# Optimization experiments

Hardware: AMD Instinct MI355X
Metric: run time of the kernel (lower is better)

## Reference

```python
import jax, jax.numpy as jnp
import numpy as np
from jax import lax

M = 4      # signature truncation depth (init kwarg m)
D = 6      # path channel dimension
L = 100000 # path length


def _kron(a, b):
    # flat tensor product of two flattened tensor levels
    return (a[:, None] * b[None, :]).ravel()


def signature(x, m):
    """Truncated path signature of x (L, d) up to depth m, flat concat of levels.
    Matches iisignature.sig(x, m): output size d + d^2 + ... + d^m.
    Sequential Chen recursion over path increments via lax.scan."""
    d = x.shape[1]
    dx = x[1:] - x[:-1]  # (L-1, d) increments

    def step(S, v):
        # exp of the linear segment: e[k] = v^{(x)k} / k!
        e = [v]
        for k in range(2, m + 1):
            e.append(_kron(e[-1], v) / k)
        # Chen: S'^k = S^k + e^k + sum_{j=1}^{k-1} S^j (x) e^{k-j}
        newS = []
        for k in range(1, m + 1):
            t = S[k - 1] + e[k - 1]
            for j in range(1, k):
                t = t + _kron(S[j - 1], e[k - 1 - j])
            newS.append(t)
        return tuple(newS), None

    S0 = tuple(jnp.zeros((d ** k,), x.dtype) for k in range(1, m + 1))
    S, _ = lax.scan(step, S0, dx)
    return jnp.concatenate(S)  # (d + d^2 + ... + d^m,)


def setup_inputs() -> dict:
    key = jax.random.key(0)
    # build a realistic path: cumulative sum of small Gaussian increments
    steps = jax.random.normal(key, (L, D), dtype=jnp.float32) * 0.01
    x = jnp.cumsum(steps, axis=0)
    return {"x": x}


def reference(x) -> jnp.ndarray:
    return signature(x, M)
```

## Files before the change

kernel.cpp:

```cpp
#include <hip/hip_runtime.h>

#define SIGSZ 1554
#define PSTRIDE 1600
#define OFF4 0
#define OFF3 1296
#define OFF2 1512
#define OFF1 1548
#define MAXROWS 80

#define REP6(M) M(0) M(1) M(2) M(3) M(4) M(5)
#define REP6B(M, k) M(k, 0) M(k, 1) M(k, 2) M(k, 3) M(k, 4) M(k, 5)
#define REP36(M) \
  REP6B(M, 0) REP6B(M, 1) REP6B(M, 2) REP6B(M, 3) REP6B(M, 4) REP6B(M, 5)

__device__ __forceinline__ float sel6(int idx, float a0, float a1, float a2,
                                      float a3, float a4, float a5) {
  float r = a0;
  r = (idx == 1) ? a1 : r;
  r = (idx == 2) ? a2 : r;
  r = (idx == 3) ? a3 : r;
  r = (idx == 4) ? a4 : r;
  r = (idx == 5) ? a5 : r;
  return r;
}

__global__ __launch_bounds__(64, 1) void sig_chunk(const float* __restrict__ x,
                                                   float* __restrict__ out,
                                                   int n_inc, int chunk_len) {
  __shared__ float xs[MAXROWS * 6];
  const int c = blockIdx.x;
  const int p = threadIdx.x;
  const int t0 = c * chunk_len;
  int t1 = t0 + chunk_len; if (t1 > n_inc) t1 = n_inc;
  const int steps = (t1 > t0) ? (t1 - t0) : 0;
  const int pc = (p < 36) ? p : 35;
  const int i = pc / 6, j = pc % 6;
  const bool act = (p < 36);

  const int nfl = (steps > 0) ? (steps + 1) * 6 : 0;
  for (int idx = p; idx < nfl; idx += 64) xs[idx] = x[(size_t)t0 * 6 + idx];
  __syncthreads();

#define DECL_S4(k, l) float s4_##k##_##l = 0.f;
  REP36(DECL_S4)
#undef DECL_S4
#define DECL_S3(k) float s3_##k = 0.f;
  REP6(DECL_S3)
#undef DECL_S3
  float s1i = 0.f, s2 = 0.f;

  float cr0 = 0, cr1 = 0, cr2 = 0, cr3 = 0, cr4 = 0, cr5 = 0;
  float nr0 = 0, nr1 = 0, nr2 = 0, nr3 = 0, nr4 = 0, nr5 = 0;
  if (steps > 0) {
    const float2* q0 = (const float2*)(xs);
    float2 a0 = q0[0], b0 = q0[1], d0 = q0[2];
    cr0 = a0.x; cr1 = a0.y; cr2 = b0.x; cr3 = b0.y; cr4 = d0.x; cr5 = d0.y;
    const float2* q1 = (const float2*)(xs + 6);
    float2 a1 = q1[0], b1 = q1[1], d1 = q1[2];
    nr0 = a1.x; nr1 = a1.y; nr2 = b1.x; nr3 = b1.y; nr4 = d1.x; nr5 = d1.y;
  }

  for (int r = 0; r < steps; ++r) {
    const float v0 = nr0 - cr0, v1 = nr1 - cr1, v2 = nr2 - cr2;
    const float v3 = nr3 - cr3, v4 = nr4 - cr4, v5 = nr5 - cr5;

    int ro = r + 2; ro = (ro > steps) ? steps : ro;
    const float2* qp = (const float2*)(xs + ro * 6);
    const float2 pa = qp[0], pb = qp[1], pd = qp[2];

    const float vi = sel6(i, v0, v1, v2, v3, v4, v5);
    const float vj = sel6(j, v0, v1, v2, v3, v4, v5);
    const float aa = vi * vj;
    const float sv = s1i * vj;
    const float G2  = fmaf(aa, 1.f / 6.f,  fmaf(sv, 0.5f,      s2));
    const float in4 = fmaf(aa, 1.f / 24.f, fmaf(sv, 1.f / 6.f, s2 * 0.5f));
#define MKG(k)                                    \
    const float G_##k = fmaf(in4, v##k, s3_##k);  \
    s3_##k = fmaf(G2, v##k, s3_##k);
    REP6(MKG)
#undef MKG
#define UPD4(k, l) s4_##k##_##l = fmaf(G_##k, v##l, s4_##k##_##l);
    REP36(UPD4)
#undef UPD4
    s2 = fmaf(fmaf(vi, 0.5f, s1i), vj, s2);
    s1i += vi;

    cr0 = nr0; cr1 = nr1; cr2 = nr2; cr3 = nr3; cr4 = nr4; cr5 = nr5;
    nr0 = pa.x; nr1 = pa.y; nr2 = pb.x; nr3 = pb.y; nr4 = pd.x; nr5 = pd.y;
  }

  float* st = out + (size_t)c * PSTRIDE;
  if (act) {
    float4* o4 = (float4*)(st + OFF4 + pc * 36);
    float4 w;
    w.x = s4_0_0; w.y = s4_0_1; w.z = s4_0_2; w.w = s4_0_3; o4[0] = w;
    w.x = s4_0_4; w.y = s4_0_5; w.z = s4_1_0; w.w = s4_1_1; o4[1] = w;
    w.x = s4_1_2; w.y = s4_1_3; w.z = s4_1_4; w.w = s4_1_5; o4[2] = w;
    w.x = s4_2_0; w.y = s4_2_1; w.z = s4_2_2; w.w = s4_2_3; o4[3] = w;
    w.x = s4_2_4; w.y = s4_2_5; w.z = s4_3_0; w.w = s4_3_1; o4[4] = w;
    w.x = s4_3_2; w.y = s4_3_3; w.z = s4_3_4; w.w = s4_3_5; o4[5] = w;
    w.x = s4_4_0; w.y = s4_4_1; w.z = s4_4_2; w.w = s4_4_3; o4[6] = w;
    w.x = s4_4_4; w.y = s4_4_5; w.z = s4_5_0; w.w = s4_5_1; o4[7] = w;
    w.x = s4_5_2; w.y = s4_5_3; w.z = s4_5_4; w.w = s4_5_5; o4[8] = w;
#define ST3(k) st[OFF3 + pc * 6 + k] = s3_##k;
    REP6(ST3)
#undef ST3
    st[OFF2 + pc] = s2;
    if (j == 0) st[OFF1 + i] = s1i;
  }
}


#define DECLSET(S)                                                  \
  float S##b4_0, S##b4_1, S##b4_2, S##b4_3, S##b4_4, S##b4_5;       \
  float S##b3r_0, S##b3r_1, S##b3r_2, S##b3r_3, S##b3r_4, S##b3r_5; \
  float S##b2r_0, S##b2r_1, S##b2r_2, S##b2r_3, S##b2r_4, S##b2r_5; \
  float S##b1_0, S##b1_1, S##b1_2, S##b1_3, S##b1_4, S##b1_5;       \
  float S##b2ij, S##b2jk, S##b3ijk, S##b1k, S##b1j;

#define LOADSET(S, bp) {                                            \
  const float2* q4 = (const float2*)((bp) + oB4);                   \
  float2 u0 = q4[0], u1 = q4[1], u2 = q4[2];                        \
  S##b4_0 = u0.x; S##b4_1 = u0.y; S##b4_2 = u1.x;                   \
  S##b4_3 = u1.y; S##b4_4 = u2.x; S##b4_5 = u2.y;                   \
  const float2* q3 = (const float2*)((bp) + oB3r);                  \
  float2 w0 = q3[0], w1 = q3[1], w2 = q3[2];                        \
  S##b3r_0 = w0.x; S##b3r_1 = w0.y; S##b3r_2 = w1.x;                \
  S##b3r_3 = w1.y; S##b3r_4 = w2.x; S##b3r_5 = w2.y;                \
  const float2* q2 = (const float2*)((bp) + oB2r);                  \
  float2 y0 = q2[0], y1 = q2[1], y2 = q2[2];                        \
  S##b2r_0 = y0.x; S##b2r_1 = y0.y; S##b2r_2 = y1.x;                \
  S##b2r_3 = y1.y; S##b2r_4 = y2.x; S##b2r_5 = y2.y;                \
  const float2* q1 = (const float2*)((bp) + OFF1);                  \
  float2 z0 = q1[0], z1 = q1[1], z2 = q1[2];                        \
  S##b1_0 = z0.x; S##b1_1 = z0.y; S##b1_2 = z1.x;                   \
  S##b1_3 = z1.y; S##b1_4 = z2.x; S##b1_5 = z2.y;                   \
  S##b2ij = (bp)[oB2ij]; S##b2jk = (bp)[oB2jk];                     \
  S##b3ijk = (bp)[oB3ijk];                                          \
  S##b1k = (bp)[oB1k]; S##b1j = (bp)[oB1j];                         \
}

#define PROD(S) {                                                   \
  const float a1i = sel6(i_, a1_0, a1_1, a1_2, a1_3, a1_4, a1_5);   \
  a4_0 = fmaf(a3, S##b1_0, fmaf(a2, S##b2r_0,                       \
         fmaf(a1i, S##b3r_0, a4_0 + S##b4_0)));                     \
  a4_1 = fmaf(a3, S##b1_1, fmaf(a2, S##b2r_1,                       \
         fmaf(a1i, S##b3r_1, a4_1 + S##b4_1)));                     \
  a4_2 = fmaf(a3, S##b1_2, fmaf(a2, S##b2r_2,                       \
         fmaf(a1i, S##b3r_2, a4_2 + S##b4_2)));                     \
  a4_3 = fmaf(a3, S##b1_3, fmaf(a2, S##b2r_3,                       \
         fmaf(a1i, S##b3r_3, a4_3 + S##b4_3)));                     \
  a4_4 = fmaf(a3, S##b1_4, fmaf(a2, S##b2r_4,                       \
         fmaf(a1i, S##b3r_4, a4_4 + S##b4_4)));                     \
  a4_5 = fmaf(a3, S##b1_5, fmaf(a2, S##b2r_5,                       \
         fmaf(a1i, S##b3r_5, a4_5 + S##b4_5)));                     \
  a3 = fmaf(a2, S##b1k, fmaf(a1i, S##b2jk, a3 + S##b3ijk));         \
  a2 = fmaf(a1i, S##b1j, a2 + S##b2ij);                             \
  a1_0 += S##b1_0; a1_1 += S##b1_1; a1_2 += S##b1_2;                \
  a1_3 += S##b1_3; a1_4 += S##b1_4; a1_5 += S##b1_5;                \
}

__global__ __launch_bounds__(256, 1) void sig_combine(const float* __restrict__ in,
                                                      float* __restrict__ out,
                                                      int n_total, int group,
                                                      int final_out) {
  const int b = blockIdx.x;
  const int p = threadIdx.x;
  const int start = b * group;
  int end = start + group; if (end > n_total) end = n_total;
  const int tc = (p < 216) ? p : 215;
  const bool act = (p < 216);
  const int k_ = tc % 6;
  const int ij = tc / 6;
  const int j_ = ij % 6;
  const int i_ = ij / 6;

  const int oB4 = OFF4 + tc * 6;
  const int oB3r = OFF3 + (j_ * 6 + k_) * 6;
  const int oB2r = OFF2 + k_ * 6;
  const int oB2ij = OFF2 + ij;
  const int oB2jk = OFF2 + j_ * 6 + k_;
  const int oB3ijk = OFF3 + tc;
  const int oB1k = OFF1 + k_;
  const int oB1j = OFF1 + j_;

  const float* sp0 = in + (size_t)start * PSTRIDE;
  float a4_0, a4_1, a4_2, a4_3, a4_4, a4_5;
  {
    const float2* q4 = (const float2*)(sp0 + oB4);
    float2 u0 = q4[0], u1 = q4[1], u2 = q4[2];
    a4_0 = u0.x; a4_1 = u0.y; a4_2 = u1.x;
    a4_3 = u1.y; a4_4 = u2.x; a4_5 = u2.y;
  }
  float a3 = sp0[oB3ijk];
  float a2 = sp0[oB2ij];
  float a1_0, a1_1, a1_2, a1_3, a1_4, a1_5;
  {
    const float2* q1 = (const float2*)(sp0 + OFF1);
    float2 z0 = q1[0], z1 = q1[1], z2 = q1[2];
    a1_0 = z0.x; a1_1 = z0.y; a1_2 = z1.x;
    a1_3 = z1.y; a1_4 = z2.x; a1_5 = z2.y;
  }

  DECLSET(A)
  DECLSET(B)

  int s = start + 1;
  {
    const int sa = (s < end) ? s : (end - 1);
    LOADSET(A, in + (size_t)sa * PSTRIDE)
    const int sb = (s + 1 < end) ? (s + 1) : (end - 1);
    LOADSET(B, in + (size_t)sb * PSTRIDE)
  }
  while (s + 1 < end) {
    PROD(A)
    {
      const int sn = (s + 2 < end) ? (s + 2) : (end - 1);
      LOADSET(A, in + (size_t)sn * PSTRIDE)
    }
    PROD(B)
    {
      const int sn = (s + 3 < end) ? (s + 3) : (end - 1);
      LOADSET(B, in + (size_t)sn * PSTRIDE)
    }
    s += 2;
  }
  if (s < end) { PROD(A) }

  const float a1p = sel6(p, a1_0, a1_1, a1_2, a1_3, a1_4, a1_5);
  if (final_out) {
    float* o = out;
    if (act) {
      float2* o2 = (float2*)(o + 258 + tc * 6);
      float2 w;
      w.x = a4_0; w.y = a4_1; o2[0] = w;
      w.x = a4_2; w.y = a4_3; o2[1] = w;
      w.x = a4_4; w.y = a4_5; o2[2] = w;
      o[42 + tc] = a3;
      if (k_ == 0) o[6 + ij] = a2;
    }
    if (p < 6) o[p] = a1p;
  } else {
    float* st = out + (size_t)b * PSTRIDE;
    if (act) {
      float2* o2 = (float2*)(st + oB4);
      float2 w;
      w.x = a4_0; w.y = a4_1; o2[0] = w;
      w.x = a4_2; w.y = a4_3; o2[1] = w;
      w.x = a4_4; w.y = a4_5; o2[2] = w;
      st[oB3ijk] = a3;
      if (k_ == 0) st[oB2ij] = a2;
    }
    if (p < 6) st[OFF1 + p] = a1p;
  }
}

extern "C" void kernel_launch(void* const* d_in, const int* in_sizes, int n_in,
                              void* d_out, int out_size, void* d_ws, size_t ws_size,
                              hipStream_t stream) {
  const float* x = (const float*)d_in[0];
  const int Lrows = in_sizes[0] / 6;
  const int n_inc = Lrows - 1;

  int P = 2048;
  int chunk_len = (n_inc + P - 1) / P;
  if (chunk_len > MAXROWS - 1) {
    chunk_len = MAXROWS - 1;
    P = (n_inc + chunk_len - 1) / chunk_len;
  }

  float* ws0 = (float*)d_ws;
  float* ws1 = ws0 + (size_t)P * PSTRIDE;

  sig_chunk<<<P, 64, 0, stream>>>(x, ws0, n_inc, chunk_len);

  float* cur = ws0;
  float* other = ws1;
  int n = P;
  while (n > 1) {
    const int g = (n <= 16) ? n : 16;
    const int nb = (n + g - 1) / g;
    const int fin = (nb == 1);
    sig_combine<<<nb, 256, 0, stream>>>(cur, fin ? (float*)d_out : other, n, g, fin);
    float* t = cur; cur = other; other = t;
    n = nb;
  }
}
```

Baseline: 94.54 us.

## Fuse combine tree into single last-block kernel and raise chunk count

Raises the chunk count from 2048 to up to 4096 with shorter chunks. The chunk kernel now precomputes increments into shared memory, unrolls the step loop by two, and allows more blocks per CU. The multi-launch combine tree becomes one kernel: each 1024-thread block combines 64 states in four subgroups merged through LDS, and the last block to finish, found with an atomic counter, combines the block results into the output. This removes several kernel launches and adds more parallel work, at the cost of atomics, fences, and the final reduction running in one block.

```diff
diff --git a/kernel.cpp b/kernel.cpp
--- a/kernel.cpp
+++ b/kernel.cpp
@@ -6,12 +6,8 @@
 #define OFF3 1296
 #define OFF2 1512
 #define OFF1 1548
-#define MAXROWS 80
-
-#define REP6(M) M(0) M(1) M(2) M(3) M(4) M(5)
-#define REP6B(M, k) M(k, 0) M(k, 1) M(k, 2) M(k, 3) M(k, 4) M(k, 5)
-#define REP36(M) \
-  REP6B(M, 0) REP6B(M, 1) REP6B(M, 2) REP6B(M, 3) REP6B(M, 4) REP6B(M, 5)
+#define VROWS 64
+#define PMAX 4096
 
 __device__ __forceinline__ float sel6(int idx, float a0, float a1, float a2,
                                       float a3, float a4, float a5) {
@@ -24,12 +20,43 @@
   return r;
 }
 
-__global__ __launch_bounds__(64, 1) void sig_chunk(const float* __restrict__ x,
+#define DECL4ROW(k) float s4_##k##_0 = 0.f, s4_##k##_1 = 0.f, s4_##k##_2 = 0.f, \
+                          s4_##k##_3 = 0.f, s4_##k##_4 = 0.f, s4_##k##_5 = 0.f;
+
+#define LOADROW(S, row) { \
+  const float2* q_ = (const float2*)(vs + (row) * 6); \
+  const float2 a_ = q_[0], b_ = q_[1], d_ = q_[2]; \
+  S##v0 = a_.x; S##v1 = a_.y; S##v2 = b_.x; \
+  S##v3 = b_.y; S##v4 = d_.x; S##v5 = d_.y; \
+  S##vi = vs[(row) * 6 + i]; S##vj = vs[(row) * 6 + j]; \
+}
+
+#define MKG_S(S, k) const float G##S##k = fmaf(in4, S##v##k, s3_##k); \
+                    s3_##k = fmaf(G2, S##v##k, s3_##k);
+#define UPD_S(S, k, l) s4_##k##_##l = fmaf(G##S##k, S##v##l, s4_##k##_##l);
+#define UPDROW_S(S, k) UPD_S(S,k,0) UPD_S(S,k,1) UPD_S(S,k,2) \
+                       UPD_S(S,k,3) UPD_S(S,k,4) UPD_S(S,k,5)
+
+#define STEP(S) { \
+  const float aa = S##vi * S##vj; \
+  const float sv = s1i * S##vj; \
+  const float G2 = fmaf(aa, 1.f / 6.f, fmaf(sv, 0.5f, s2)); \
+  const float in4 = fmaf(aa, 1.f / 24.f, fmaf(sv, 1.f / 6.f, s2 * 0.5f)); \
+  MKG_S(S,0) MKG_S(S,1) MKG_S(S,2) MKG_S(S,3) MKG_S(S,4) MKG_S(S,5) \
+  UPDROW_S(S,0) UPDROW_S(S,1) UPDROW_S(S,2) \
+  UPDROW_S(S,3) UPDROW_S(S,4) UPDROW_S(S,5) \
+  s2 = fmaf(fmaf(S##vi, 0.5f, s1i), S##vj, s2); \
+  s1i += S##vi; \
+}
+
+__global__ __launch_bounds__(64, 4) void sig_chunk(const float* __restrict__ x,
                                                    float* __restrict__ out,
+                                                   unsigned* __restrict__ counter,
                                                    int n_inc, int chunk_len) {
-  __shared__ float xs[MAXROWS * 6];
+  __shared__ alignas(16) float vs[VROWS * 6];
   const int c = blockIdx.x;
   const int p = threadIdx.x;
+  if (c == 0 && p == 0) *counter = 0u;
   const int t0 = c * chunk_len;
   int t1 = t0 + chunk_len; if (t1 > n_inc) t1 = n_inc;
   const int steps = (t1 > t0) ? (t1 - t0) : 0;
@@ -37,56 +64,26 @@
   const int i = pc / 6, j = pc % 6;
   const bool act = (p < 36);
 
-  const int nfl = (steps > 0) ? (steps + 1) * 6 : 0;
-  for (int idx = p; idx < nfl; idx += 64) xs[idx] = x[(size_t)t0 * 6 + idx];
+  const int nv = steps * 6;
+  const float* xb = x + (size_t)t0 * 6;
+  for (int idx = p; idx < nv; idx += 64) vs[idx] = xb[idx + 6] - xb[idx];
+  for (int idx = nv + p; idx < nv + 18; idx += 64) vs[idx] = 0.f;
   __syncthreads();
 
-#define DECL_S4(k, l) float s4_##k##_##l = 0.f;
-  REP36(DECL_S4)
-#undef DECL_S4
-#define DECL_S3(k) float s3_##k = 0.f;
-  REP6(DECL_S3)
-#undef DECL_S3
+  DECL4ROW(0) DECL4ROW(1) DECL4ROW(2) DECL4ROW(3) DECL4ROW(4) DECL4ROW(5)
+  float s3_0 = 0.f, s3_1 = 0.f, s3_2 = 0.f, s3_3 = 0.f, s3_4 = 0.f, s3_5 = 0.f;
   float s1i = 0.f, s2 = 0.f;
 
-  float cr0 = 0, cr1 = 0, cr2 = 0, cr3 = 0, cr4 = 0, cr5 = 0;
-  float nr0 = 0, nr1 = 0, nr2 = 0, nr3 = 0, nr4 = 0, nr5 = 0;
-  if (steps > 0) {
-    const float2* q0 = (const float2*)(xs);
-    float2 a0 = q0[0], b0 = q0[1], d0 = q0[2];
-    cr0 = a0.x; cr1 = a0.y; cr2 = b0.x; cr3 = b0.y; cr4 = d0.x; cr5 = d0.y;
-    const float2* q1 = (const float2*)(xs + 6);
-    float2 a1 = q1[0], b1 = q1[1], d1 = q1[2];
-    nr0 = a1.x; nr1 = a1.y; nr2 = b1.x; nr3 = b1.y; nr4 = d1.x; nr5 = d1.y;
-  }
-
-  for (int r = 0; r < steps; ++r) {
-    const float v0 = nr0 - cr0, v1 = nr1 - cr1, v2 = nr2 - cr2;
-    const float v3 = nr3 - cr3, v4 = nr4 - cr4, v5 = nr5 - cr5;
-
-    int ro = r + 2; ro = (ro > steps) ? steps : ro;
-    const float2* qp = (const float2*)(xs + ro * 6);
-    const float2 pa = qp[0], pb = qp[1], pd = qp[2];
-
-    const float vi = sel6(i, v0, v1, v2, v3, v4, v5);
-    const float vj = sel6(j, v0, v1, v2, v3, v4, v5);
-    const float aa = vi * vj;
-    const float sv = s1i * vj;
-    const float G2  = fmaf(aa, 1.f / 6.f,  fmaf(sv, 0.5f,      s2));
-    const float in4 = fmaf(aa, 1.f / 24.f, fmaf(sv, 1.f / 6.f, s2 * 0.5f));
-#define MKG(k)                                    \
-    const float G_##k = fmaf(in4, v##k, s3_##k);  \
-    s3_##k = fmaf(G2, v##k, s3_##k);
-    REP6(MKG)
-#undef MKG
-#define UPD4(k, l) s4_##k##_##l = fmaf(G_##k, v##l, s4_##k##_##l);
-    REP36(UPD4)
-#undef UPD4
-    s2 = fmaf(fmaf(vi, 0.5f, s1i), vj, s2);
-    s1i += vi;
-
-    cr0 = nr0; cr1 = nr1; cr2 = nr2; cr3 = nr3; cr4 = nr4; cr5 = nr5;
-    nr0 = pa.x; nr1 = pa.y; nr2 = pb.x; nr3 = pb.y; nr4 = pd.x; nr5 = pd.y;
+  float Av0, Av1, Av2, Av3, Av4, Av5, Avi, Avj;
+  float Bv0, Bv1, Bv2, Bv3, Bv4, Bv5, Bvi, Bvj;
+  LOADROW(A, 0)
+  LOADROW(B, 1)
+  const int steps_up = (steps + 1) & ~1;
+  for (int r = 0; r < steps_up; r += 2) {
+    STEP(A)
+    LOADROW(A, r + 2)
+    STEP(B)
+    LOADROW(B, r + 3)
   }
 
   float* st = out + (size_t)c * PSTRIDE;
@@ -102,14 +99,44 @@
     w.x = s4_4_0; w.y = s4_4_1; w.z = s4_4_2; w.w = s4_4_3; o4[6] = w;
     w.x = s4_4_4; w.y = s4_4_5; w.z = s4_5_0; w.w = s4_5_1; o4[7] = w;
     w.x = s4_5_2; w.y = s4_5_3; w.z = s4_5_4; w.w = s4_5_5; o4[8] = w;
-#define ST3(k) st[OFF3 + pc * 6 + k] = s3_##k;
-    REP6(ST3)
-#undef ST3
+    st[OFF3 + pc * 6 + 0] = s3_0;
+    st[OFF3 + pc * 6 + 1] = s3_1;
+    st[OFF3 + pc * 6 + 2] = s3_2;
+    st[OFF3 + pc * 6 + 3] = s3_3;
+    st[OFF3 + pc * 6 + 4] = s3_4;
+    st[OFF3 + pc * 6 + 5] = s3_5;
     st[OFF2 + pc] = s2;
     if (j == 0) st[OFF1 + i] = s1i;
   }
 }
 
+struct Acc {
+  float a4_0, a4_1, a4_2, a4_3, a4_4, a4_5;
+  float a3, a2;
+  float a1_0, a1_1, a1_2, a1_3, a1_4, a1_5;
+};
+
+struct Lane {
+  int i_, j_, k_, ij, tc;
+  int oB4, oB3r, oB2r, oB2ij, oB2jk, oB3ijk, oB1k, oB1j;
+  bool act;
+};
+
+__device__ __forceinline__ Lane make_lane(int pl) {
+  Lane L;
+  const int tc = (pl < 216) ? pl : 215;
+  L.tc = tc; L.act = (pl < 216);
+  L.k_ = tc % 6; L.ij = tc / 6; L.j_ = L.ij % 6; L.i_ = L.ij / 6;
+  L.oB4 = OFF4 + tc * 6;
+  L.oB3r = OFF3 + (L.j_ * 6 + L.k_) * 6;
+  L.oB2r = OFF2 + L.k_ * 6;
+  L.oB2ij = OFF2 + L.ij;
+  L.oB2jk = OFF2 + L.j_ * 6 + L.k_;
+  L.oB3ijk = OFF3 + tc;
+  L.oB1k = OFF1 + L.k_;
+  L.oB1j = OFF1 + L.j_;
+  return L;
+}
 
 #define DECLSET(S)                                                  \
   float S##b4_0, S##b4_1, S##b4_2, S##b4_3, S##b4_4, S##b4_5;       \
@@ -119,139 +146,175 @@
   float S##b2ij, S##b2jk, S##b3ijk, S##b1k, S##b1j;
 
 #define LOADSET(S, bp) {                                            \
-  const float2* q4 = (const float2*)((bp) + oB4);                   \
-  float2 u0 = q4[0], u1 = q4[1], u2 = q4[2];                        \
+  const float2* q4 = (const float2*)((bp) + L.oB4);                 \
+  const float2 u0 = q4[0], u1 = q4[1], u2 = q4[2];                  \
   S##b4_0 = u0.x; S##b4_1 = u0.y; S##b4_2 = u1.x;                   \
   S##b4_3 = u1.y; S##b4_4 = u2.x; S##b4_5 = u2.y;                   \
-  const float2* q3 = (const float2*)((bp) + oB3r);                  \
-  float2 w0 = q3[0], w1 = q3[1], w2 = q3[2];                        \
+  const float2* q3 = (const float2*)((bp) + L.oB3r);                \
+  const float2 w0 = q3[0], w1 = q3[1], w2 = q3[2];                  \
   S##b3r_0 = w0.x; S##b3r_1 = w0.y; S##b3r_2 = w1.x;                \
   S##b3r_3 = w1.y; S##b3r_4 = w2.x; S##b3r_5 = w2.y;                \
-  const float2* q2 = (const float2*)((bp) + oB2r);                  \
-  float2 y0 = q2[0], y1 = q2[1], y2 = q2[2];                        \
+  const float2* q2 = (const float2*)((bp) + L.oB2r);                \
+  const float2 y0 = q2[0], y1 = q2[1], y2 = q2[2];                  \
   S##b2r_0 = y0.x; S##b2r_1 = y0.y; S##b2r_2 = y1.x;                \
   S##b2r_3 = y1.y; S##b2r_4 = y2.x; S##b2r_5 = y2.y;                \
   const float2* q1 = (const float2*)((bp) + OFF1);                  \
-  float2 z0 = q1[0], z1 = q1[1], z2 = q1[2];                        \
+  const float2 z0 = q1[0], z1 = q1[1], z2 = q1[2];                  \
   S##b1_0 = z0.x; S##b1_1 = z0.y; S##b1_2 = z1.x;                   \
   S##b1_3 = z1.y; S##b1_4 = z2.x; S##b1_5 = z2.y;                   \
-  S##b2ij = (bp)[oB2ij]; S##b2jk = (bp)[oB2jk];                     \
-  S##b3ijk = (bp)[oB3ijk];                                          \
-  S##b1k = (bp)[oB1k]; S##b1j = (bp)[oB1j];                         \
+  S##b2ij = (bp)[L.oB2ij]; S##b2jk = (bp)[L.oB2jk];                 \
+  S##b3ijk = (bp)[L.oB3ijk];                                        \
+  S##b1k = (bp)[L.oB1k]; S##b1j = (bp)[L.oB1j];                     \
 }
 
 #define PROD(S) {                                                   \
-  const float a1i = sel6(i_, a1_0, a1_1, a1_2, a1_3, a1_4, a1_5);   \
-  a4_0 = fmaf(a3, S##b1_0, fmaf(a2, S##b2r_0,                       \
-         fmaf(a1i, S##b3r_0, a4_0 + S##b4_0)));                     \
-  a4_1 = fmaf(a3, S##b1_1, fmaf(a2, S##b2r_1,                       \
-         fmaf(a1i, S##b3r_1, a4_1 + S##b4_1)));                     \
-  a4_2 = fmaf(a3, S##b1_2, fmaf(a2, S##b2r_2,                       \
-         fmaf(a1i, S##b3r_2, a4_2 + S##b4_2)));                     \
-  a4_3 = fmaf(a3, S##b1_3, fmaf(a2, S##b2r_3,                       \
-         fmaf(a1i, S##b3r_3, a4_3 + S##b4_3)));                     \
-  a4_4 = fmaf(a3, S##b1_4, fmaf(a2, S##b2r_4,                       \
-         fmaf(a1i, S##b3r_4, a4_4 + S##b4_4)));                     \
-  a4_5 = fmaf(a3, S##b1_5, fmaf(a2, S##b2r_5,                       \
-         fmaf(a1i, S##b3r_5, a4_5 + S##b4_5)));                     \
-  a3 = fmaf(a2, S##b1k, fmaf(a1i, S##b2jk, a3 + S##b3ijk));         \
-  a2 = fmaf(a1i, S##b1j, a2 + S##b2ij);                             \
-  a1_0 += S##b1_0; a1_1 += S##b1_1; a1_2 += S##b1_2;                \
-  a1_3 += S##b1_3; a1_4 += S##b1_4; a1_5 += S##b1_5;                \
-}
-
-__global__ __launch_bounds__(256, 1) void sig_combine(const float* __restrict__ in,
-                                                      float* __restrict__ out,
-                                                      int n_total, int group,
-                                                      int final_out) {
-  const int b = blockIdx.x;
-  const int p = threadIdx.x;
-  const int start = b * group;
-  int end = start + group; if (end > n_total) end = n_total;
-  const int tc = (p < 216) ? p : 215;
-  const bool act = (p < 216);
-  const int k_ = tc % 6;
-  const int ij = tc / 6;
-  const int j_ = ij % 6;
-  const int i_ = ij / 6;
-
-  const int oB4 = OFF4 + tc * 6;
-  const int oB3r = OFF3 + (j_ * 6 + k_) * 6;
-  const int oB2r = OFF2 + k_ * 6;
-  const int oB2ij = OFF2 + ij;
-  const int oB2jk = OFF2 + j_ * 6 + k_;
-  const int oB3ijk = OFF3 + tc;
-  const int oB1k = OFF1 + k_;
-  const int oB1j = OFF1 + j_;
-
-  const float* sp0 = in + (size_t)start * PSTRIDE;
-  float a4_0, a4_1, a4_2, a4_3, a4_4, a4_5;
+  const float a1i = sel6(L.i_, acc.a1_0, acc.a1_1, acc.a1_2,        \
+                         acc.a1_3, acc.a1_4, acc.a1_5);             \
+  acc.a4_0 = fmaf(acc.a3, S##b1_0, fmaf(acc.a2, S##b2r_0,           \
+             fmaf(a1i, S##b3r_0, acc.a4_0 + S##b4_0)));             \
+  acc.a4_1 = fmaf(acc.a3, S##b1_1, fmaf(acc.a2, S##b2r_1,           \
+             fmaf(a1i, S##b3r_1, acc.a4_1 + S##b4_1)));             \
+  acc.a4_2 = fmaf(acc.a3, S##b1_2, fmaf(acc.a2, S##b2r_2,           \
+             fmaf(a1i, S##b3r_2, acc.a4_2 + S##b4_2)));             \
+  acc.a4_3 = fmaf(acc.a3, S##b1_3, fmaf(acc.a2, S##b2r_3,           \
+             fmaf(a1i, S##b3r_3, acc.a4_3 + S##b4_3)));             \
+  acc.a4_4 = fmaf(acc.a3, S##b1_4, fmaf(acc.a2, S##b2r_4,           \
+             fmaf(a1i, S##b3r_4, acc.a4_4 + S##b4_4)));             \
+  acc.a4_5 = fmaf(acc.a3, S##b1_5, fmaf(acc.a2, S##b2r_5,           \
+             fmaf(a1i, S##b3r_5, acc.a4_5 + S##b4_5)));             \
+  acc.a3 = fmaf(acc.a2, S##b1k, fmaf(a1i, S##b2jk, acc.a3 + S##b3ijk)); \
+  acc.a2 = fmaf(a1i, S##b1j, acc.a2 + S##b2ij);                     \
+  acc.a1_0 += S##b1_0; acc.a1_1 += S##b1_1; acc.a1_2 += S##b1_2;    \
+  acc.a1_3 += S##b1_3; acc.a1_4 += S##b1_4; acc.a1_5 += S##b1_5;    \
+}
+
+__device__ __forceinline__ Acc combine_span(const float* base, int first,
+                                            int cnt, const Lane& L) {
+  Acc acc = {};
+  if (cnt <= 0) return acc;
+  const float* sp0 = base + (size_t)first * PSTRIDE;
   {
-    const float2* q4 = (const float2*)(sp0 + oB4);
-    float2 u0 = q4[0], u1 = q4[1], u2 = q4[2];
-    a4_0 = u0.x; a4_1 = u0.y; a4_2 = u1.x;
-    a4_3 = u1.y; a4_4 = u2.x; a4_5 = u2.y;
-  }
-  float a3 = sp0[oB3ijk];
-  float a2 = sp0[oB2ij];
-  float a1_0, a1_1, a1_2, a1_3, a1_4, a1_5;
+    const float2* q4 = (const float2*)(sp0 + L.oB4);
+    const float2 u0 = q4[0], u1 = q4[1], u2 = q4[2];
+    acc.a4_0 = u0.x; acc.a4_1 = u0.y; acc.a4_2 = u1.x;
+    acc.a4_3 = u1.y; acc.a4_4 = u2.x; acc.a4_5 = u2.y;
+    acc.a3 = sp0[L.oB3ijk];
+    acc.a2 = sp0[L.oB2ij];
+    const float2* q1 = (const float2*)(sp0 + OFF1);
+    const float2 z0 = q1[0], z1 = q1[1], z2 = q1[2];
+    acc.a1_0 = z0.x; acc.a1_1 = z0.y; acc.a1_2 = z1.x;
+    acc.a1_3 = z1.y; acc.a1_4 = z2.x; acc.a1_5 = z2.y;
+  }
+  if (cnt == 1) return acc;
+  DECLSET(X)
+  DECLSET(Y)
+  const int end = first + cnt;
+  int s = first + 1;
   {
-    const float2* q1 = (const float2*)(sp0 + OFF1);
-    float2 z0 = q1[0], z1 = q1[1], z2 = q1[2];
-    a1_0 = z0.x; a1_1 = z0.y; a1_2 = z1.x;
-    a1_3 = z1.y; a1_4 = z2.x; a1_5 = z2.y;
-  }
-
-  DECLSET(A)
-  DECLSET(B)
-
-  int s = start + 1;
-  {
-    const int sa = (s < end) ? s : (end - 1);
-    LOADSET(A, in + (size_t)sa * PSTRIDE)
+    LOADSET(X, base + (size_t)s * PSTRIDE)
     const int sb = (s + 1 < end) ? (s + 1) : (end - 1);
-    LOADSET(B, in + (size_t)sb * PSTRIDE)
+    LOADSET(Y, base + (size_t)sb * PSTRIDE)
   }
   while (s + 1 < end) {
-    PROD(A)
+    PROD(X)
     {
       const int sn = (s + 2 < end) ? (s + 2) : (end - 1);
-      LOADSET(A, in + (size_t)sn * PSTRIDE)
+      LOADSET(X, base + (size_t)sn * PSTRIDE)
     }
-    PROD(B)
+    PROD(Y)
     {
       const int sn = (s + 3 < end) ? (s + 3) : (end - 1);
-      LOADSET(B, in + (size_t)sn * PSTRIDE)
+      LOADSET(Y, base + (size_t)sn * PSTRIDE)
     }
     s += 2;
   }
-  if (s < end) { PROD(A) }
-
-  const float a1p = sel6(p, a1_0, a1_1, a1_2, a1_3, a1_4, a1_5);
-  if (final_out) {
-    float* o = out;
-    if (act) {
-      float2* o2 = (float2*)(o + 258 + tc * 6);
-      float2 w;
-      w.x = a4_0; w.y = a4_1; o2[0] = w;
-      w.x = a4_2; w.y = a4_3; o2[1] = w;
-      w.x = a4_4; w.y = a4_5; o2[2] = w;
-      o[42 + tc] = a3;
-      if (k_ == 0) o[6 + ij] = a2;
+  if (s < end) { PROD(X) }
+  return acc;
+}
+
+__device__ __forceinline__ void apply_state(Acc& acc, const float* bp,
+                                            const Lane& L) {
+  DECLSET(Z)
+  LOADSET(Z, bp)
+  PROD(Z)
+}
+
+__device__ __forceinline__ void store_partial(float* st, const Acc& acc,
+                                              const Lane& L, int pl) {
+  if (L.act) {
+    float2* o2 = (float2*)(st + L.oB4);
+    float2 w;
+    w.x = acc.a4_0; w.y = acc.a4_1; o2[0] = w;
+    w.x = acc.a4_2; w.y = acc.a4_3; o2[1] = w;
+    w.x = acc.a4_4; w.y = acc.a4_5; o2[2] = w;
+    st[L.oB3ijk] = acc.a3;
+    if (L.k_ == 0) st[L.oB2ij] = acc.a2;
+  }
+  if (pl < 6)
+    st[OFF1 + pl] = sel6(pl, acc.a1_0, acc.a1_1, acc.a1_2,
+                         acc.a1_3, acc.a1_4, acc.a1_5);
+}
+
+__device__ __forceinline__ void store_final(float* o, const Acc& acc,
+                                            const Lane& L, int pl) {
+  if (L.act) {
+    float2* o2 = (float2*)(o + 258 + L.tc * 6);
+    float2 w;
+    w.x = acc.a4_0; w.y = acc.a4_1; o2[0] = w;
+    w.x = acc.a4_2; w.y = acc.a4_3; o2[1] = w;
+    w.x = acc.a4_4; w.y = acc.a4_5; o2[2] = w;
+    o[42 + L.tc] = acc.a3;
+    if (L.k_ == 0) o[6 + L.ij] = acc.a2;
+  }
+  if (pl < 6)
+    o[pl] = sel6(pl, acc.a1_0, acc.a1_1, acc.a1_2,
+                 acc.a1_3, acc.a1_4, acc.a1_5);
+}
+
+__global__ __launch_bounds__(1024) void sig_combine_all(
+    const float* __restrict__ in, float* __restrict__ mid,
+    float* __restrict__ out, unsigned* __restrict__ counter, int n_total) {
+  __shared__ alignas(16) float lds[3 * PSTRIDE];
+  __shared__ unsigned s_last;
+  const int pl = threadIdx.x & 255;
+  const int sub = threadIdx.x >> 8;
+  const Lane L = make_lane(pl);
+
+  {
+    const int gs = blockIdx.x * 64 + sub * 16;
+    int gc = n_total - gs; if (gc > 16) gc = 16;
+    Acc acc = combine_span(in, gs, gc, L);
+    if (sub != 0) store_partial(lds + (size_t)(sub - 1) * PSTRIDE, acc, L, pl);
+    __syncthreads();
+    if (sub == 0) {
+      apply_state(acc, lds + 0 * PSTRIDE, L);
+      apply_state(acc, lds + 1 * PSTRIDE, L);
+      apply_state(acc, lds + 2 * PSTRIDE, L);
+      store_partial(mid + (size_t)blockIdx.x * PSTRIDE, acc, L, pl);
     }
-    if (p < 6) o[p] = a1p;
-  } else {
-    float* st = out + (size_t)b * PSTRIDE;
-    if (act) {
-      float2* o2 = (float2*)(st + oB4);
-      float2 w;
-      w.x = a4_0; w.y = a4_1; o2[0] = w;
-      w.x = a4_2; w.y = a4_3; o2[1] = w;
-      w.x = a4_4; w.y = a4_5; o2[2] = w;
-      st[oB3ijk] = a3;
-      if (k_ == 0) st[oB2ij] = a2;
+  }
+
+  __threadfence();
+  __syncthreads();
+  if (threadIdx.x == 0)
+    s_last = (atomicAdd(counter, 1u) == (unsigned)(gridDim.x - 1)) ? 1u : 0u;
+  __syncthreads();
+  if (!s_last) return;
+  __threadfence();
+
+  {
+    const int gs = sub * 16;
+    int gc = (int)gridDim.x - gs; if (gc > 16) gc = 16;
+    Acc acc = combine_span(mid, gs, gc, L);
+    __syncthreads();
+    if (sub != 0) store_partial(lds + (size_t)(sub - 1) * PSTRIDE, acc, L, pl);
+    __syncthreads();
+    if (sub == 0) {
+      apply_state(acc, lds + 0 * PSTRIDE, L);
+      apply_state(acc, lds + 1 * PSTRIDE, L);
+      apply_state(acc, lds + 2 * PSTRIDE, L);
+      store_final(out, acc, L, pl);
     }
-    if (p < 6) st[OFF1 + p] = a1p;
   }
 }
 
@@ -262,27 +325,19 @@
   const int Lrows = in_sizes[0] / 6;
   const int n_inc = Lrows - 1;
 
-  int P = 2048;
+  int P = PMAX;
   int chunk_len = (n_inc + P - 1) / P;
-  if (chunk_len > MAXROWS - 1) {
-    chunk_len = MAXROWS - 1;
+  if (chunk_len > VROWS - 3) {
+    chunk_len = VROWS - 3;
     P = (n_inc + chunk_len - 1) / chunk_len;
   }
 
   float* ws0 = (float*)d_ws;
-  float* ws1 = ws0 + (size_t)P * PSTRIDE;
-
-  sig_chunk<<<P, 64, 0, stream>>>(x, ws0, n_inc, chunk_len);
-
-  float* cur = ws0;
-  float* other = ws1;
-  int n = P;
-  while (n > 1) {
-    const int g = (n <= 16) ? n : 16;
-    const int nb = (n + g - 1) / g;
-    const int fin = (nb == 1);
-    sig_combine<<<nb, 256, 0, stream>>>(cur, fin ? (float*)d_out : other, n, g, fin);
-    float* t = cur; cur = other; other = t;
-    n = nb;
-  }
-}
+  float* ws1 = ws0 + (size_t)PMAX * PSTRIDE;
+  unsigned* counter = (unsigned*)(ws1 + (size_t)64 * PSTRIDE);
+
+  sig_chunk<<<P, 64, 0, stream>>>(x, ws0, counter, n_inc, chunk_len);
+
+  const int nb = (P + 63) / 64;
+  sig_combine_all<<<nb, 1024, 0, stream>>>(ws0, ws1, (float*)d_out, counter, P);
+}
```

After: 135.5 us. +43.3%, slower.

## Vectorize chunk kernel with packed float2 FMAs, precomputed increments, more chunks

Applied to the files above, without the earlier changes.

The chunk kernel now computes increments once into shared memory and updates the level-3 and level-4 accumulators with packed two-wide FMAs. It also replaces the six-way select with direct LDS indexing and unrolls the step loop by two using double-buffered row loads. The chunk count doubles from 2048 to 4096 so chunks are shorter, and launch bounds allow four blocks per unit. The aim is fewer VALU instructions per step and more parallelism, paid for with a larger combine tree and more partial-signature traffic through the workspace.

```diff
diff --git a/kernel.cpp b/kernel.cpp
--- a/kernel.cpp
+++ b/kernel.cpp
@@ -6,12 +6,17 @@
 #define OFF3 1296
 #define OFF2 1512
 #define OFF1 1548
-#define MAXROWS 80
-
-#define REP6(M) M(0) M(1) M(2) M(3) M(4) M(5)
-#define REP6B(M, k) M(k, 0) M(k, 1) M(k, 2) M(k, 3) M(k, 4) M(k, 5)
-#define REP36(M) \
-  REP6B(M, 0) REP6B(M, 1) REP6B(M, 2) REP6B(M, 3) REP6B(M, 4) REP6B(M, 5)
+#define VROWS 64
+#define PMAX 4096
+
+typedef float v2f __attribute__((ext_vector_type(2)));
+
+__device__ __forceinline__ v2f vfma2(v2f a, v2f b, v2f c) {
+  return __builtin_elementwise_fma(a, b, c);
+}
+__device__ __forceinline__ v2f splat2(float s) {
+  v2f r; r.x = s; r.y = s; return r;
+}
 
 __device__ __forceinline__ float sel6(int idx, float a0, float a1, float a2,
                                       float a3, float a4, float a5) {
@@ -24,10 +29,44 @@
   return r;
 }
 
-__global__ __launch_bounds__(64, 1) void sig_chunk(const float* __restrict__ x,
+#define DECL4ROW(k) v2f s4_##k##_0 = {0.f, 0.f}, s4_##k##_1 = {0.f, 0.f}, \
+                        s4_##k##_2 = {0.f, 0.f};
+
+#define LOADROW(S, row) { \
+  const v2f* q_ = (const v2f*)(vs + (row) * 6); \
+  S##p0 = q_[0]; S##p1 = q_[1]; S##p2 = q_[2]; \
+  S##vi = vs[(row) * 6 + i]; S##vj = vs[(row) * 6 + j]; \
+}
+
+#define UPD4K(S, k, gk) { \
+  const v2f gk2 = splat2(gk); \
+  s4_##k##_0 = vfma2(gk2, S##p0, s4_##k##_0); \
+  s4_##k##_1 = vfma2(gk2, S##p1, s4_##k##_1); \
+  s4_##k##_2 = vfma2(gk2, S##p2, s4_##k##_2); \
+}
+
+#define STEP(S) { \
+  const float aa = S##vi * S##vj; \
+  const float sv = s1i * S##vj; \
+  const float G2 = fmaf(aa, 1.f / 6.f, fmaf(sv, 0.5f, s2)); \
+  const float in4 = fmaf(aa, 1.f / 24.f, fmaf(sv, 1.f / 6.f, s2 * 0.5f)); \
+  const v2f in42 = splat2(in4), G22 = splat2(G2); \
+  const v2f Gp0 = vfma2(in42, S##p0, s3p0); \
+  const v2f Gp1 = vfma2(in42, S##p1, s3p1); \
+  const v2f Gp2 = vfma2(in42, S##p2, s3p2); \
+  s3p0 = vfma2(G22, S##p0, s3p0); \
+  s3p1 = vfma2(G22, S##p1, s3p1); \
+  s3p2 = vfma2(G22, S##p2, s3p2); \
+  UPD4K(S, 0, Gp0.x) UPD4K(S, 1, Gp0.y) UPD4K(S, 2, Gp1.x) \
+  UPD4K(S, 3, Gp1.y) UPD4K(S, 4, Gp2.x) UPD4K(S, 5, Gp2.y) \
+  s2 = fmaf(fmaf(S##vi, 0.5f, s1i), S##vj, s2); \
+  s1i += S##vi; \
+}
+
+__global__ __launch_bounds__(64, 4) void sig_chunk(const float* __restrict__ x,
                                                    float* __restrict__ out,
                                                    int n_inc, int chunk_len) {
-  __shared__ float xs[MAXROWS * 6];
+  __shared__ alignas(16) float vs[VROWS * 6];
   const int c = blockIdx.x;
   const int p = threadIdx.x;
   const int t0 = c * chunk_len;
@@ -37,74 +76,47 @@
   const int i = pc / 6, j = pc % 6;
   const bool act = (p < 36);
 
-  const int nfl = (steps > 0) ? (steps + 1) * 6 : 0;
-  for (int idx = p; idx < nfl; idx += 64) xs[idx] = x[(size_t)t0 * 6 + idx];
+  const int nv = steps * 6;
+  const float* xb = x + (size_t)t0 * 6;
+  for (int idx = p; idx < nv; idx += 64) vs[idx] = xb[idx + 6] - xb[idx];
+  for (int idx = nv + p; idx < nv + 18; idx += 64) vs[idx] = 0.f;
   __syncthreads();
 
-#define DECL_S4(k, l) float s4_##k##_##l = 0.f;
-  REP36(DECL_S4)
-#undef DECL_S4
-#define DECL_S3(k) float s3_##k = 0.f;
-  REP6(DECL_S3)
-#undef DECL_S3
+  DECL4ROW(0) DECL4ROW(1) DECL4ROW(2) DECL4ROW(3) DECL4ROW(4) DECL4ROW(5)
+  v2f s3p0 = {0.f, 0.f}, s3p1 = {0.f, 0.f}, s3p2 = {0.f, 0.f};
   float s1i = 0.f, s2 = 0.f;
 
-  float cr0 = 0, cr1 = 0, cr2 = 0, cr3 = 0, cr4 = 0, cr5 = 0;
-  float nr0 = 0, nr1 = 0, nr2 = 0, nr3 = 0, nr4 = 0, nr5 = 0;
-  if (steps > 0) {
-    const float2* q0 = (const float2*)(xs);
-    float2 a0 = q0[0], b0 = q0[1], d0 = q0[2];
-    cr0 = a0.x; cr1 = a0.y; cr2 = b0.x; cr3 = b0.y; cr4 = d0.x; cr5 = d0.y;
-    const float2* q1 = (const float2*)(xs + 6);
-    float2 a1 = q1[0], b1 = q1[1], d1 = q1[2];
-    nr0 = a1.x; nr1 = a1.y; nr2 = b1.x; nr3 = b1.y; nr4 = d1.x; nr5 = d1.y;
-  }
-
-  for (int r = 0; r < steps; ++r) {
-    const float v0 = nr0 - cr0, v1 = nr1 - cr1, v2 = nr2 - cr2;
-    const float v3 = nr3 - cr3, v4 = nr4 - cr4, v5 = nr5 - cr5;
-
-    int ro = r + 2; ro = (ro > steps) ? steps : ro;
-    const float2* qp = (const float2*)(xs + ro * 6);
-    const float2 pa = qp[0], pb = qp[1], pd = qp[2];
-
-    const float vi = sel6(i, v0, v1, v2, v3, v4, v5);
-    const float vj = sel6(j, v0, v1, v2, v3, v4, v5);
-    const float aa = vi * vj;
-    const float sv = s1i * vj;
-    const float G2  = fmaf(aa, 1.f / 6.f,  fmaf(sv, 0.5f,      s2));
-    const float in4 = fmaf(aa, 1.f / 24.f, fmaf(sv, 1.f / 6.f, s2 * 0.5f));
-#define MKG(k)                                    \
-    const float G_##k = fmaf(in4, v##k, s3_##k);  \
-    s3_##k = fmaf(G2, v##k, s3_##k);
-    REP6(MKG)
-#undef MKG
-#define UPD4(k, l) s4_##k##_##l = fmaf(G_##k, v##l, s4_##k##_##l);
-    REP36(UPD4)
-#undef UPD4
-    s2 = fmaf(fmaf(vi, 0.5f, s1i), vj, s2);
-    s1i += vi;
-
-    cr0 = nr0; cr1 = nr1; cr2 = nr2; cr3 = nr3; cr4 = nr4; cr5 = nr5;
-    nr0 = pa.x; nr1 = pa.y; nr2 = pb.x; nr3 = pb.y; nr4 = pd.x; nr5 = pd.y;
+  v2f Ap0, Ap1, Ap2; float Avi, Avj;
+  v2f Bp0, Bp1, Bp2; float Bvi, Bvj;
+  LOADROW(A, 0)
+  LOADROW(B, 1)
+  const int steps_up = (steps + 1) & ~1;
+  for (int r = 0; r < steps_up; r += 2) {
+    STEP(A)
+    LOADROW(A, r + 2)
+    STEP(B)
+    LOADROW(B, r + 3)
   }
 
   float* st = out + (size_t)c * PSTRIDE;
   if (act) {
     float4* o4 = (float4*)(st + OFF4 + pc * 36);
     float4 w;
-    w.x = s4_0_0; w.y = s4_0_1; w.z = s4_0_2; w.w = s4_0_3; o4[0] = w;
-    w.x = s4_0_4; w.y = s4_0_5; w.z = s4_1_0; w.w = s4_1_1; o4[1] = w;
-    w.x = s4_1_2; w.y = s4_1_3; w.z = s4_1_4; w.w = s4_1_5; o4[2] = w;
-    w.x = s4_2_0; w.y = s4_2_1; w.z = s4_2_2; w.w = s4_2_3; o4[3] = w;
-    w.x = s4_2_4; w.y = s4_2_5; w.z = s4_3_0; w.w = s4_3_1; o4[4] = w;
-    w.x = s4_3_2; w.y = s4_3_3; w.z = s4_3_4; w.w = s4_3_5; o4[5] = w;
-    w.x = s4_4_0; w.y = s4_4_1; w.z = s4_4_2; w.w = s4_4_3; o4[6] = w;
-    w.x = s4_4_4; w.y = s4_4_5; w.z = s4_5_0; w.w = s4_5_1; o4[7] = w;
-    w.x = s4_5_2; w.y = s4_5_3; w.z = s4_5_4; w.w = s4_5_5; o4[8] = w;
-#define ST3(k) st[OFF3 + pc * 6 + k] = s3_##k;
-    REP6(ST3)
-#undef ST3
+    w.x = s4_0_0.x; w.y = s4_0_0.y; w.z = s4_0_1.x; w.w = s4_0_1.y; o4[0] = w;
+    w.x = s4_0_2.x; w.y = s4_0_2.y; w.z = s4_1_0.x; w.w = s4_1_0.y; o4[1] = w;
+    w.x = s4_1_1.x; w.y = s4_1_1.y; w.z = s4_1_2.x; w.w = s4_1_2.y; o4[2] = w;
+    w.x = s4_2_0.x; w.y = s4_2_0.y; w.z = s4_2_1.x; w.w = s4_2_1.y; o4[3] = w;
+    w.x = s4_2_2.x; w.y = s4_2_2.y; w.z = s4_3_0.x; w.w = s4_3_0.y; o4[4] = w;
+    w.x = s4_3_1.x; w.y = s4_3_1.y; w.z = s4_3_2.x; w.w = s4_3_2.y; o4[5] = w;
+    w.x = s4_4_0.x; w.y = s4_4_0.y; w.z = s4_4_1.x; w.w = s4_4_1.y; o4[6] = w;
+    w.x = s4_4_2.x; w.y = s4_4_2.y; w.z = s4_5_0.x; w.w = s4_5_0.y; o4[7] = w;
+    w.x = s4_5_1.x; w.y = s4_5_1.y; w.z = s4_5_2.x; w.w = s4_5_2.y; o4[8] = w;
+    st[OFF3 + pc * 6 + 0] = s3p0.x;
+    st[OFF3 + pc * 6 + 1] = s3p0.y;
+    st[OFF3 + pc * 6 + 2] = s3p1.x;
+    st[OFF3 + pc * 6 + 3] = s3p1.y;
+    st[OFF3 + pc * 6 + 4] = s3p2.x;
+    st[OFF3 + pc * 6 + 5] = s3p2.y;
     st[OFF2 + pc] = s2;
     if (j == 0) st[OFF1 + i] = s1i;
   }
@@ -262,15 +274,15 @@
   const int Lrows = in_sizes[0] / 6;
   const int n_inc = Lrows - 1;
 
-  int P = 2048;
+  int P = PMAX;
   int chunk_len = (n_inc + P - 1) / P;
-  if (chunk_len > MAXROWS - 1) {
-    chunk_len = MAXROWS - 1;
+  if (chunk_len > VROWS - 3) {
+    chunk_len = VROWS - 3;
     P = (n_inc + chunk_len - 1) / chunk_len;
   }
 
   float* ws0 = (float*)d_ws;
-  float* ws1 = ws0 + (size_t)P * PSTRIDE;
+  float* ws1 = ws0 + (size_t)PMAX * PSTRIDE;
 
   sig_chunk<<<P, 64, 0, stream>>>(x, ws0, n_inc, chunk_len);
 
```

Result: slower. 98.42 us (+4.1%).
